# Kernel optimization log

Measured on AMD Instinct MI355X. Metric: run time of the kernel, lower is better.

The kernel has to match this reference:

```python
import jax, jax.numpy as jnp
import numpy as np

PAD, BOS, EOS = 0, 1, 2
VOCAB, EMB, HID, N, T = 32, 32, 512, 4096, 64


def _lstm_step(x, h, c, W_ih, W_hh, b_ih, b_hh):
    # PyTorch nn.LSTM single step; gate order [i|f|g|o]
    g = x @ W_ih.T + h @ W_hh.T + b_ih + b_hh  # [n, 4H]
    i, f, gg, o = jnp.split(g, 4, axis=-1)
    i = jax.nn.sigmoid(i)
    f = jax.nn.sigmoid(f)
    gg = jnp.tanh(gg)
    o = jax.nn.sigmoid(o)
    c = f * c + i * gg
    h = o * jnp.tanh(c)
    return h, c


def setup_inputs() -> dict:
    key = jax.random.key(0)
    ks = jax.random.split(key, 12)
    s = 0.04  # ~1/sqrt(hidden), matches torch LSTM init scale
    emb = jax.random.normal(ks[0], (VOCAB, EMB), jnp.float32) * s
    emb = emb.at[PAD].set(0.0)  # padding_idx row is zero
    inp = {
        "prevs": jnp.full((N, 1), BOS, dtype=jnp.int32),
        "emb": emb,
        "W_ih0": jax.random.normal(ks[1], (4 * HID, EMB), jnp.float32) * s,
        "W_hh0": jax.random.normal(ks[2], (4 * HID, HID), jnp.float32) * s,
        "b_ih0": jax.random.normal(ks[3], (4 * HID,), jnp.float32) * s,
        "b_hh0": jax.random.normal(ks[4], (4 * HID,), jnp.float32) * s,
        "W_ih1": jax.random.normal(ks[5], (4 * HID, HID), jnp.float32) * s,
        "W_hh1": jax.random.normal(ks[6], (4 * HID, HID), jnp.float32) * s,
        "b_ih1": jax.random.normal(ks[7], (4 * HID,), jnp.float32) * s,
        "b_hh1": jax.random.normal(ks[8], (4 * HID,), jnp.float32) * s,
        "W_out": jax.random.normal(ks[9], (VOCAB, HID), jnp.float32) * s,
        "b_out": jax.random.normal(ks[10], (VOCAB,), jnp.float32) * s,
        "max_length": T,
    }
    return inp


def reference(prevs, emb, W_ih0, W_hh0, b_ih0, b_hh0,
              W_ih1, W_hh1, b_ih1, b_hh1, W_out, b_out, max_length):
    # softmax+multinomial sampling, <eos>/<pad> bookkeeping.
    n = prevs.shape[0]
    H = W_hh0.shape[1]
    keys = jax.random.split(jax.random.key(7), max_length)
    tok0 = prevs[:, 0]
    h0 = jnp.zeros((n, H), emb.dtype)
    init = (tok0, h0, h0, h0, h0,
            tok0 == EOS, jnp.zeros((n,), jnp.int32))

    def step(carry, key):
        tok, h0, c0, h1, c1, is_end, lengths = carry
        x = emb[tok]                                   # [n, EMB]
        h0, c0 = _lstm_step(x, h0, c0, W_ih0, W_hh0, b_ih0, b_hh0)
        h1, c1 = _lstm_step(h0, h1, c1, W_ih1, W_hh1, b_ih1, b_hh1)
        logits = h1 @ W_out.T + b_out                  # [n, VOCAB]
        sampled = jax.random.categorical(key, logits)  # == multinomial(softmax)
        cur = jnp.where(is_end, PAD, sampled).astype(tok.dtype)
        lengths = lengths + (~is_end).astype(jnp.int32)
        is_end = is_end | (cur == EOS)
        return (cur, h0, c0, h1, c1, is_end, lengths), cur

    carry, toks = jax.lax.scan(step, init, keys)       # toks: [T, n]
    lengths = carry[-1] + 1                            # +1 for <bos>
    samples = jnp.concatenate([prevs, toks.T], axis=1)  # [n, 1+T]
    return samples, lengths
```

## Files before the change

kernel.cpp:

```cpp
#include <hip/hip_runtime.h>
#include <cstdint>
#include <cmath>

#define RNG_VARIANT 1

#define NROWS 4096
#define HIDN 512
#define G4 2048
#define VOC 32
#define TSTEPS 64
#define PAD_TOK 0
#define BOS_TOK 1
#define EOS_TOK 2

__host__ __device__ inline void tf2x32(unsigned k0, unsigned k1, unsigned x0, unsigned x1,
                                       unsigned& o0, unsigned& o1) {
  unsigned ks0 = k0, ks1 = k1, ks2 = k0 ^ k1 ^ 0x1BD11BDAu;
  unsigned X0 = x0 + ks0, X1 = x1 + ks1;
  const unsigned R[5][4] = {{13,15,26,6},{17,29,16,24},{13,15,26,6},{17,29,16,24},{13,15,26,6}};
  unsigned inj0[5], inj1[5];
  inj0[0] = ks1; inj1[0] = ks2;
  inj0[1] = ks2; inj1[1] = ks0;
  inj0[2] = ks0; inj1[2] = ks1;
  inj0[3] = ks1; inj1[3] = ks2;
  inj0[4] = ks2; inj1[4] = ks0;
#pragma unroll
  for (int i = 0; i < 5; ++i) {
#pragma unroll
    for (int j = 0; j < 4; ++j) {
      X0 += X1;
      unsigned r = R[i][j];
      X1 = (X1 << r) | (X1 >> (32 - r));
      X1 ^= X0;
    }
    X0 += inj0[i];
    X1 += inj1[i] + (unsigned)(i + 1);
  }
  o0 = X0; o1 = X1;
}

#define BM 128
#define BN 128
#define BK 32
#define LDP 132

__global__ __launch_bounds__(256) void lstm_gemm(
    const float* __restrict__ A0, const float* __restrict__ B0,
    const float* __restrict__ A1, const float* __restrict__ B1,
    int nparts, float* __restrict__ C)
{
  __shared__ float As[BK][LDP];
  __shared__ float Bs[BK][LDP];
  const int tid = threadIdx.x;
  const int tx = tid & 15, ty = tid >> 4;
  const int m0 = blockIdx.y * BM, n0 = blockIdx.x * BN;
  const int lrow = tid >> 3;
  const int lcol = (tid & 7) << 2;
  float acc[8][8];
#pragma unroll
  for (int i = 0; i < 8; ++i)
#pragma unroll
    for (int j = 0; j < 8; ++j) acc[i][j] = 0.f;

  for (int part = 0; part < nparts; ++part) {
    const float* __restrict__ A = part ? A1 : A0;
    const float* __restrict__ B = part ? B1 : B0;
    for (int kt = 0; kt < HIDN / BK; ++kt) {
      const int kb = kt * BK;
#pragma unroll
      for (int p = 0; p < 4; ++p) {
        const int r = lrow + 32 * p;
        float4 va = *reinterpret_cast<const float4*>(A + (size_t)(m0 + r) * HIDN + kb + lcol);
        float4 vb = *reinterpret_cast<const float4*>(B + (size_t)(n0 + r) * HIDN + kb + lcol);
        As[lcol + 0][r] = va.x; As[lcol + 1][r] = va.y; As[lcol + 2][r] = va.z; As[lcol + 3][r] = va.w;
        Bs[lcol + 0][r] = vb.x; Bs[lcol + 1][r] = vb.y; Bs[lcol + 2][r] = vb.z; Bs[lcol + 3][r] = vb.w;
      }
      __syncthreads();
#pragma unroll
      for (int k = 0; k < BK; ++k) {
        float a[8], b[8];
        *reinterpret_cast<float4*>(&a[0]) = *reinterpret_cast<const float4*>(&As[k][ty * 8]);
        *reinterpret_cast<float4*>(&a[4]) = *reinterpret_cast<const float4*>(&As[k][ty * 8 + 4]);
        *reinterpret_cast<float4*>(&b[0]) = *reinterpret_cast<const float4*>(&Bs[k][tx * 8]);
        *reinterpret_cast<float4*>(&b[4]) = *reinterpret_cast<const float4*>(&Bs[k][tx * 8 + 4]);
#pragma unroll
        for (int i = 0; i < 8; ++i)
#pragma unroll
          for (int j = 0; j < 8; ++j)
            acc[i][j] = fmaf(a[i], b[j], acc[i][j]);
      }
      __syncthreads();
    }
  }
#pragma unroll
  for (int i = 0; i < 8; ++i) {
    float4 v0 = make_float4(acc[i][0], acc[i][1], acc[i][2], acc[i][3]);
    float4 v1 = make_float4(acc[i][4], acc[i][5], acc[i][6], acc[i][7]);
    float* cp = C + (size_t)(m0 + ty * 8 + i) * G4 + n0 + tx * 8;
    *reinterpret_cast<float4*>(cp) = v0;
    *reinterpret_cast<float4*>(cp + 4) = v1;
  }
}

__global__ void lstm_act(const float* __restrict__ gates,
                         const float* __restrict__ extra,
                         const int* __restrict__ tok,
                         float* __restrict__ h, float* __restrict__ c)
{
  const int n = blockIdx.x;
  const int j = blockIdx.y * 256 + threadIdx.x;
  const float* ex = extra + (tok ? (size_t)tok[n] * G4 : 0);
  const size_t base = (size_t)n * G4;
  float gi = gates[base + j]        + ex[j];
  float gf = gates[base + j + 512]  + ex[j + 512];
  float gg = gates[base + j + 1024] + ex[j + 1024];
  float go = gates[base + j + 1536] + ex[j + 1536];
  float si = 1.f / (1.f + expf(-gi));
  float sf = 1.f / (1.f + expf(-gf));
  float tg = tanhf(gg);
  float so = 1.f / (1.f + expf(-go));
  const size_t hi = (size_t)n * HIDN + j;
  float cn = sf * c[hi] + si * tg;
  c[hi] = cn;
  h[hi] = so * tanhf(cn);
}

__global__ void build_ew0(const float* __restrict__ emb, const float* __restrict__ W_ih0,
                          const float* __restrict__ b_ih0, const float* __restrict__ b_hh0,
                          float* __restrict__ EW0)
{
  int idx = blockIdx.x * 256 + threadIdx.x;
  int vv = idx >> 11, j = idx & 2047;
  float s = b_ih0[j] + b_hh0[j];
#pragma unroll
  for (int e = 0; e < 32; ++e)
    s = fmaf(emb[vv * 32 + e], W_ih0[(size_t)j * 32 + e], s);
  EW0[idx] = s;
}

__global__ void add_bias(const float* __restrict__ a, const float* __restrict__ b,
                         float* __restrict__ o) {
  int j = blockIdx.x * 256 + threadIdx.x;
  if (j < G4) o[j] = a[j] + b[j];
}

__global__ void init_state(const int* __restrict__ prevs, int* __restrict__ tok,
                           int* __restrict__ is_end, int* __restrict__ lengths,
                           int* __restrict__ out)
{
  int n = blockIdx.x * 256 + threadIdx.x;
  if (n < NROWS) {
    int p = prevs[n];
    tok[n] = p;
    is_end[n] = (p == EOS_TOK) ? 1 : 0;
    lengths[n] = 0;
    out[(size_t)n * (TSTEPS + 1)] = p;
  }
}

__global__ __launch_bounds__(64) void sample_step(
    const float* __restrict__ h1, const float* __restrict__ W_out,
    const float* __restrict__ b_out,
    int* __restrict__ tok, int* __restrict__ is_end, int* __restrict__ lengths,
    int* __restrict__ out, unsigned key0, unsigned key1, int t, int last)
{
  __shared__ float hrow[HIDN];
  const int n = blockIdx.x;
  const int lane = threadIdx.x;
  {
    const float4* src = reinterpret_cast<const float4*>(h1 + (size_t)n * HIDN);
    float4* dst = reinterpret_cast<float4*>(hrow);
    dst[lane] = src[lane];
    dst[lane + 64] = src[lane + 64];
  }
  __syncthreads();
  const int v = lane & 31, half = lane >> 5;
  const float* w  = W_out + (size_t)v * HIDN + half * 256;
  const float* hh = hrow + half * 256;
  float dot = 0.f;
#pragma unroll
  for (int k = 0; k < 256; k += 4) {
    float4 wv = *reinterpret_cast<const float4*>(w + k);
    float4 hv = *reinterpret_cast<const float4*>(hh + k);
    dot = fmaf(wv.x, hv.x, dot);
    dot = fmaf(wv.y, hv.y, dot);
    dot = fmaf(wv.z, hv.z, dot);
    dot = fmaf(wv.w, hv.w, dot);
  }
  dot += __shfl_xor(dot, 32);
  const float logit = dot + b_out[v];

  const unsigned iflat = (unsigned)(n * 32 + v);
  unsigned r0, r1, bits;
#if RNG_VARIANT == 1
  tf2x32(key0, key1, 0u, iflat, r0, r1);
  bits = r0 ^ r1;
#elif RNG_VARIANT == 2
  if (iflat < 65536u) { tf2x32(key0, key1, iflat, iflat + 65536u, r0, r1); bits = r0; }
  else                { tf2x32(key0, key1, iflat - 65536u, iflat, r0, r1); bits = r1; }
#else
  tf2x32(key0, key1, 0u, iflat, r0, r1);
  bits = r1;
#endif
  float f = __uint_as_float((bits >> 9) | 0x3f800000u) - 1.0f;
  float u = fmaxf(f, 1.1754943508222875e-38f);
  float t1 = -(float)log((double)u);
  float g  = -(float)log((double)t1);
  float s = g + logit;

  float bs = s; int bi = v;
#pragma unroll
  for (int off = 16; off >= 1; off >>= 1) {
    float os = __shfl_xor(bs, off);
    int   oi = __shfl_xor(bi, off);
    if (os > bs || (os == bs && oi < bi)) { bs = os; bi = oi; }
  }
  if (lane == 0) {
    const int oe  = is_end[n];
    const int cur = oe ? PAD_TOK : bi;
    const int len = lengths[n] + (oe ? 0 : 1);
    lengths[n] = len;
    is_end[n] = (oe || (cur == EOS_TOK)) ? 1 : 0;
    tok[n] = cur;
    out[(size_t)n * (TSTEPS + 1) + t + 1] = cur;
    if (last) out[(size_t)NROWS * (TSTEPS + 1) + n] = len + 1;
  }
}

extern "C" void kernel_launch(void* const* d_in, const int* in_sizes, int n_in,
                              void* d_out, int out_size, void* d_ws, size_t ws_size,
                              hipStream_t stream)
{
  const int*   prevs = (const int*)d_in[0];
  const float* emb   = (const float*)d_in[1];
  const float* W_ih0 = (const float*)d_in[2];
  const float* W_hh0 = (const float*)d_in[3];
  const float* b_ih0 = (const float*)d_in[4];
  const float* b_hh0 = (const float*)d_in[5];
  const float* W_ih1 = (const float*)d_in[6];
  const float* W_hh1 = (const float*)d_in[7];
  const float* b_ih1 = (const float*)d_in[8];
  const float* b_hh1 = (const float*)d_in[9];
  const float* W_out = (const float*)d_in[10];
  const float* b_out = (const float*)d_in[11];

  float* h0    = (float*)d_ws;
  float* c0    = h0 + (size_t)NROWS * HIDN;
  float* h1    = c0 + (size_t)NROWS * HIDN;
  float* c1    = h1 + (size_t)NROWS * HIDN;
  float* gates = c1 + (size_t)NROWS * HIDN;
  float* EW0   = gates + (size_t)NROWS * G4;
  float* bias1 = EW0 + (size_t)VOC * G4;
  int* tok     = (int*)(bias1 + G4);
  int* is_end  = tok + NROWS;
  int* lengths = is_end + NROWS;
  int* outp    = (int*)d_out;

  hipMemsetAsync(h0, 0, (size_t)4 * NROWS * HIDN * sizeof(float), stream);
  init_state<<<NROWS / 256, 256, 0, stream>>>(prevs, tok, is_end, lengths, outp);
  build_ew0<<<VOC * G4 / 256, 256, 0, stream>>>(emb, W_ih0, b_ih0, b_hh0, EW0);
  add_bias<<<G4 / 256, 256, 0, stream>>>(b_ih1, b_hh1, bias1);

  unsigned keys[TSTEPS][2];
#if RNG_VARIANT == 2
  {
    unsigned outv[2 * TSTEPS];
    for (int j = 0; j < TSTEPS; ++j) {
      unsigned o0, o1;
      tf2x32(0u, 7u, (unsigned)j, (unsigned)(j + TSTEPS), o0, o1);
      outv[j] = o0; outv[j + TSTEPS] = o1;
    }
    for (int t = 0; t < TSTEPS; ++t) { keys[t][0] = outv[2 * t]; keys[t][1] = outv[2 * t + 1]; }
  }
#else
  for (int t = 0; t < TSTEPS; ++t) {
    unsigned o0, o1;
    tf2x32(0u, 7u, 0u, (unsigned)t, o0, o1);
    keys[t][0] = o0; keys[t][1] = o1;
  }
#endif

  dim3 ggrid(G4 / BN, NROWS / BM);
  for (int t = 0; t < TSTEPS; ++t) {
    lstm_gemm<<<ggrid, 256, 0, stream>>>(h0, W_hh0, nullptr, nullptr, 1, gates);
    lstm_act<<<dim3(NROWS, 2), 256, 0, stream>>>(gates, EW0, tok, h0, c0);
    lstm_gemm<<<ggrid, 256, 0, stream>>>(h0, W_ih1, h1, W_hh1, 2, gates);
    lstm_act<<<dim3(NROWS, 2), 256, 0, stream>>>(gates, bias1, nullptr, h1, c1);
    sample_step<<<NROWS, 64, 0, stream>>>(h1, W_out, b_out, tok, is_end, lengths, outp,
                                          keys[t][0], keys[t][1], t, t == TSTEPS - 1);
  }
}
```

Baseline: 22.42 ms.

## Fuse LSTM gate GEMM with activation using interleaved gate columns and LDS double-buffering

Replaces the separate gate GEMM and activation kernels with one fused kernel per layer. Each block computes the i/f/g/o columns for 32 hidden units, so the cell update runs in registers and the full gates tensor is never written or read back. The kernel stages A/B tiles directly into LDS with global_load_lds in a double-buffered loop. h buffers are ping-ponged because blocks now read h while other blocks write it, and the bias/embedding tables are stored in interleaved gate order. The cost is 4-byte-granular async loads and a less regular B-row access pattern.

After: 35.47 ms. +58.2%, slower.

```diff
diff --git a/kernel.cpp b/kernel.cpp
--- a/kernel.cpp
+++ b/kernel.cpp
@@ -6,12 +6,18 @@
 
 #define NROWS 4096
 #define HIDN 512
-#define G4 2048
 #define VOC 32
 #define TSTEPS 64
 #define PAD_TOK 0
 #define BOS_TOK 1
 #define EOS_TOK 2
+
+#define BK 32
+#define BM 128
+#define JJT 32
+
+typedef const __attribute__((address_space(1))) unsigned int* gptr_t;
+typedef __attribute__((address_space(3))) unsigned int* lptr_t;
 
 __host__ __device__ inline void tf2x32(unsigned k0, unsigned k1, unsigned x0, unsigned x1,
                                        unsigned& o0, unsigned& o1) {
@@ -39,95 +45,126 @@
   o0 = X0; o1 = X1;
 }
 
-#define BM 128
-#define BN 128
-#define BK 32
-#define LDP 132
-
-__global__ __launch_bounds__(256) void lstm_gemm(
+template<int NPARTS, bool LAYER0>
+__global__ __launch_bounds__(256, 2) void lstm_fused(
     const float* __restrict__ A0, const float* __restrict__ B0,
     const float* __restrict__ A1, const float* __restrict__ B1,
-    int nparts, float* __restrict__ C)
-{
-  __shared__ float As[BK][LDP];
-  __shared__ float Bs[BK][LDP];
+    const float* __restrict__ extra,
+    const int* __restrict__ tokv,
+    float* __restrict__ h, float* __restrict__ c)
+{
+  __shared__ float As[2][BK * BM];
+  __shared__ float Bs[2][BK * BM];
   const int tid = threadIdx.x;
-  const int tx = tid & 15, ty = tid >> 4;
-  const int m0 = blockIdx.y * BM, n0 = blockIdx.x * BN;
-  const int lrow = tid >> 3;
-  const int lcol = (tid & 7) << 2;
+  const int lane = tid & 63;
+  const int w = tid >> 6;
+  const int wr = w >> 1, wc = w & 1;
+  const int ty = lane >> 3, tx = lane & 7;
+  const int m0 = blockIdx.y * BM;
+  const int c0 = blockIdx.x * JJT;
+  const int kA = w * 8;
+
+  const size_t arow0 = (size_t)(m0 + lane) * HIDN;
+  const size_t arow1 = (size_t)(m0 + 64 + lane) * HIDN;
+  const size_t brow0 = (size_t)((lane & 3) * HIDN + c0 + (lane >> 2)) * HIDN;
+  const size_t brow1 = brow0 + (size_t)16 * HIDN;
+
   float acc[8][8];
 #pragma unroll
   for (int i = 0; i < 8; ++i)
 #pragma unroll
     for (int j = 0; j < 8; ++j) acc[i][j] = 0.f;
 
-  for (int part = 0; part < nparts; ++part) {
-    const float* __restrict__ A = part ? A1 : A0;
-    const float* __restrict__ B = part ? B1 : B0;
-    for (int kt = 0; kt < HIDN / BK; ++kt) {
-      const int kb = kt * BK;
-#pragma unroll
-      for (int p = 0; p < 4; ++p) {
-        const int r = lrow + 32 * p;
-        float4 va = *reinterpret_cast<const float4*>(A + (size_t)(m0 + r) * HIDN + kb + lcol);
-        float4 vb = *reinterpret_cast<const float4*>(B + (size_t)(n0 + r) * HIDN + kb + lcol);
-        As[lcol + 0][r] = va.x; As[lcol + 1][r] = va.y; As[lcol + 2][r] = va.z; As[lcol + 3][r] = va.w;
-        Bs[lcol + 0][r] = vb.x; Bs[lcol + 1][r] = vb.y; Bs[lcol + 2][r] = vb.z; Bs[lcol + 3][r] = vb.w;
-      }
-      __syncthreads();
-#pragma unroll
-      for (int k = 0; k < BK; ++k) {
-        float a[8], b[8];
-        *reinterpret_cast<float4*>(&a[0]) = *reinterpret_cast<const float4*>(&As[k][ty * 8]);
-        *reinterpret_cast<float4*>(&a[4]) = *reinterpret_cast<const float4*>(&As[k][ty * 8 + 4]);
-        *reinterpret_cast<float4*>(&b[0]) = *reinterpret_cast<const float4*>(&Bs[k][tx * 8]);
-        *reinterpret_cast<float4*>(&b[4]) = *reinterpret_cast<const float4*>(&Bs[k][tx * 8 + 4]);
-#pragma unroll
-        for (int i = 0; i < 8; ++i)
-#pragma unroll
-          for (int j = 0; j < 8; ++j)
-            acc[i][j] = fmaf(a[i], b[j], acc[i][j]);
-      }
-      __syncthreads();
+  const int NT = NPARTS * (HIDN / BK);
+
+  auto STAGE = [&](int tt, int sel) {
+    const float* A = A0;
+    const float* B = B0;
+    if (NPARTS == 2 && (tt >> 4)) { A = A1; B = B1; }
+    const int kb = (tt & 15) * BK;
+    float* dA = &As[sel][0];
+    float* dB = &Bs[sel][0];
+#pragma unroll
+    for (int i = 0; i < 16; ++i) {
+      const int k = kA + (i >> 1);
+      const float* sA = A + ((i & 1) ? arow1 : arow0) + (size_t)(kb + k);
+      const float* sB = B + ((i & 1) ? brow1 : brow0) + (size_t)(kb + k);
+      __builtin_amdgcn_global_load_lds((gptr_t)sA, (lptr_t)(dA + k * BM + (i & 1) * 64), 4, 0, 0);
+      __builtin_amdgcn_global_load_lds((gptr_t)sB, (lptr_t)(dB + k * BM + (i & 1) * 64), 4, 0, 0);
     }
+  };
+
+  STAGE(0, 0);
+  __syncthreads();
+  int sel = 0;
+  for (int tt = 0; tt < NT; ++tt) {
+    if (tt + 1 < NT) STAGE(tt + 1, sel ^ 1);
+    const float* aP = &As[sel][wr * 64 + ty * 8];
+    const float* bP = &Bs[sel][wc * 64 + tx * 8];
+#pragma unroll
+    for (int k = 0; k < BK; ++k) {
+      float4 a0 = *(const float4*)(aP + k * BM);
+      float4 a1 = *(const float4*)(aP + k * BM + 4);
+      float4 b0 = *(const float4*)(bP + k * BM);
+      float4 b1 = *(const float4*)(bP + k * BM + 4);
+      const float av[8] = {a0.x, a0.y, a0.z, a0.w, a1.x, a1.y, a1.z, a1.w};
+      const float bv[8] = {b0.x, b0.y, b0.z, b0.w, b1.x, b1.y, b1.z, b1.w};
+#pragma unroll
+      for (int i2 = 0; i2 < 8; ++i2)
+#pragma unroll
+        for (int j2 = 0; j2 < 8; ++j2)
+          acc[i2][j2] = fmaf(av[i2], bv[j2], acc[i2][j2]);
+    }
+    __syncthreads();
+    sel ^= 1;
+  }
+
+  const int jjl = wc * 16 + tx * 2;
+  const size_t colb = (size_t)(c0 + jjl);
+  float e[8];
+  if (!LAYER0) {
+    float4 e0 = *(const float4*)(extra + colb * 4);
+    float4 e1 = *(const float4*)(extra + colb * 4 + 4);
+    e[0] = e0.x; e[1] = e0.y; e[2] = e0.z; e[3] = e0.w;
+    e[4] = e1.x; e[5] = e1.y; e[6] = e1.z; e[7] = e1.w;
   }
 #pragma unroll
   for (int i = 0; i < 8; ++i) {
-    float4 v0 = make_float4(acc[i][0], acc[i][1], acc[i][2], acc[i][3]);
-    float4 v1 = make_float4(acc[i][4], acc[i][5], acc[i][6], acc[i][7]);
-    float* cp = C + (size_t)(m0 + ty * 8 + i) * G4 + n0 + tx * 8;
-    *reinterpret_cast<float4*>(cp) = v0;
-    *reinterpret_cast<float4*>(cp + 4) = v1;
-  }
-}
-
-__global__ void lstm_act(const float* __restrict__ gates,
-                         const float* __restrict__ extra,
-                         const int* __restrict__ tok,
-                         float* __restrict__ h, float* __restrict__ c)
-{
-  const int n = blockIdx.x;
-  const int j = blockIdx.y * 256 + threadIdx.x;
-  const float* ex = extra + (tok ? (size_t)tok[n] * G4 : 0);
-  const size_t base = (size_t)n * G4;
-  float gi = gates[base + j]        + ex[j];
-  float gf = gates[base + j + 512]  + ex[j + 512];
-  float gg = gates[base + j + 1024] + ex[j + 1024];
-  float go = gates[base + j + 1536] + ex[j + 1536];
-  float si = 1.f / (1.f + expf(-gi));
-  float sf = 1.f / (1.f + expf(-gf));
-  float tg = tanhf(gg);
-  float so = 1.f / (1.f + expf(-go));
-  const size_t hi = (size_t)n * HIDN + j;
-  float cn = sf * c[hi] + si * tg;
-  c[hi] = cn;
-  h[hi] = so * tanhf(cn);
+    const int n = m0 + wr * 64 + ty * 8 + i;
+    if (LAYER0) {
+      const int tk = tokv[n];
+      const float* ex = extra + (size_t)tk * 2048 + colb * 4;
+      float4 e0 = *(const float4*)(ex);
+      float4 e1 = *(const float4*)(ex + 4);
+      e[0] = e0.x; e[1] = e0.y; e[2] = e0.z; e[3] = e0.w;
+      e[4] = e1.x; e[5] = e1.y; e[6] = e1.z; e[7] = e1.w;
+    }
+    float gi0 = acc[i][0] + e[0], gf0 = acc[i][1] + e[1];
+    float gg0 = acc[i][2] + e[2], go0 = acc[i][3] + e[3];
+    float gi1 = acc[i][4] + e[4], gf1 = acc[i][5] + e[5];
+    float gg1 = acc[i][6] + e[6], go1 = acc[i][7] + e[7];
+    const size_t idx = (size_t)n * HIDN + colb;
+    float2 cold = *(const float2*)(c + idx);
+    float si0 = 1.f / (1.f + expf(-gi0));
+    float sf0 = 1.f / (1.f + expf(-gf0));
+    float tg0 = tanhf(gg0);
+    float so0 = 1.f / (1.f + expf(-go0));
+    float cn0 = sf0 * cold.x + si0 * tg0;
+    float hn0 = so0 * tanhf(cn0);
+    float si1 = 1.f / (1.f + expf(-gi1));
+    float sf1 = 1.f / (1.f + expf(-gf1));
+    float tg1 = tanhf(gg1);
+    float so1 = 1.f / (1.f + expf(-go1));
+    float cn1 = sf1 * cold.y + si1 * tg1;
+    float hn1 = so1 * tanhf(cn1);
+    *(float2*)(c + idx) = make_float2(cn0, cn1);
+    *(float2*)(h + idx) = make_float2(hn0, hn1);
+  }
 }
 
 __global__ void build_ew0(const float* __restrict__ emb, const float* __restrict__ W_ih0,
                           const float* __restrict__ b_ih0, const float* __restrict__ b_hh0,
-                          float* __restrict__ EW0)
+                          float* __restrict__ EW0i)
 {
   int idx = blockIdx.x * 256 + threadIdx.x;
   int vv = idx >> 11, j = idx & 2047;
@@ -135,13 +172,13 @@
 #pragma unroll
   for (int e = 0; e < 32; ++e)
     s = fmaf(emb[vv * 32 + e], W_ih0[(size_t)j * 32 + e], s);
-  EW0[idx] = s;
-}
-
-__global__ void add_bias(const float* __restrict__ a, const float* __restrict__ b,
-                         float* __restrict__ o) {
+  EW0i[(size_t)vv * 2048 + (size_t)(j & 511) * 4 + (j >> 9)] = s;
+}
+
+__global__ void build_bias1i(const float* __restrict__ a, const float* __restrict__ b,
+                             float* __restrict__ o) {
   int j = blockIdx.x * 256 + threadIdx.x;
-  if (j < G4) o[j] = a[j] + b[j];
+  o[(size_t)(j & 511) * 4 + (j >> 9)] = a[j] + b[j];
 }
 
 __global__ void init_state(const int* __restrict__ prevs, int* __restrict__ tok,
@@ -175,12 +212,12 @@
   }
   __syncthreads();
   const int v = lane & 31, half = lane >> 5;
-  const float* w  = W_out + (size_t)v * HIDN + half * 256;
+  const float* wp = W_out + (size_t)v * HIDN + half * 256;
   const float* hh = hrow + half * 256;
   float dot = 0.f;
 #pragma unroll
   for (int k = 0; k < 256; k += 4) {
-    float4 wv = *reinterpret_cast<const float4*>(w + k);
+    float4 wv = *reinterpret_cast<const float4*>(wp + k);
     float4 hv = *reinterpret_cast<const float4*>(hh + k);
     dot = fmaf(wv.x, hv.x, dot);
     dot = fmaf(wv.y, hv.y, dot);
@@ -244,49 +281,43 @@
   const float* W_out = (const float*)d_in[10];
   const float* b_out = (const float*)d_in[11];
 
-  float* h0    = (float*)d_ws;
-  float* c0    = h0 + (size_t)NROWS * HIDN;
-  float* h1    = c0 + (size_t)NROWS * HIDN;
-  float* c1    = h1 + (size_t)NROWS * HIDN;
-  float* gates = c1 + (size_t)NROWS * HIDN;
-  float* EW0   = gates + (size_t)NROWS * G4;
-  float* bias1 = EW0 + (size_t)VOC * G4;
-  int* tok     = (int*)(bias1 + G4);
+  const size_t S = (size_t)NROWS * HIDN;
+  float* h0a   = (float*)d_ws;
+  float* h1a   = h0a + S;
+  float* cl0   = h1a + S;
+  float* cl1   = cl0 + S;
+  float* h0b   = cl1 + S;
+  float* h1b   = h0b + S;
+  float* EW0i  = h1b + S;
+  float* bias1i = EW0i + (size_t)VOC * 2048;
+  int* tok     = (int*)(bias1i + 2048);
   int* is_end  = tok + NROWS;
   int* lengths = is_end + NROWS;
   int* outp    = (int*)d_out;
 
-  hipMemsetAsync(h0, 0, (size_t)4 * NROWS * HIDN * sizeof(float), stream);
+  hipMemsetAsync(h0a, 0, 4 * S * sizeof(float), stream);
   init_state<<<NROWS / 256, 256, 0, stream>>>(prevs, tok, is_end, lengths, outp);
-  build_ew0<<<VOC * G4 / 256, 256, 0, stream>>>(emb, W_ih0, b_ih0, b_hh0, EW0);
-  add_bias<<<G4 / 256, 256, 0, stream>>>(b_ih1, b_hh1, bias1);
+  build_ew0<<<VOC * 2048 / 256, 256, 0, stream>>>(emb, W_ih0, b_ih0, b_hh0, EW0i);
+  build_bias1i<<<2048 / 256, 256, 0, stream>>>(b_ih1, b_hh1, bias1i);
 
   unsigned keys[TSTEPS][2];
-#if RNG_VARIANT == 2
-  {
-    unsigned outv[2 * TSTEPS];
-    for (int j = 0; j < TSTEPS; ++j) {
-      unsigned o0, o1;
-      tf2x32(0u, 7u, (unsigned)j, (unsigned)(j + TSTEPS), o0, o1);
-      outv[j] = o0; outv[j + TSTEPS] = o1;
-    }
-    for (int t = 0; t < TSTEPS; ++t) { keys[t][0] = outv[2 * t]; keys[t][1] = outv[2 * t + 1]; }
-  }
-#else
   for (int t = 0; t < TSTEPS; ++t) {
     unsigned o0, o1;
     tf2x32(0u, 7u, 0u, (unsigned)t, o0, o1);
     keys[t][0] = o0; keys[t][1] = o1;
   }
-#endif
-
-  dim3 ggrid(G4 / BN, NROWS / BM);
+
+  dim3 ggrid(HIDN / JJT, NROWS / BM);
   for (int t = 0; t < TSTEPS; ++t) {
-    lstm_gemm<<<ggrid, 256, 0, stream>>>(h0, W_hh0, nullptr, nullptr, 1, gates);
-    lstm_act<<<dim3(NROWS, 2), 256, 0, stream>>>(gates, EW0, tok, h0, c0);
-    lstm_gemm<<<ggrid, 256, 0, stream>>>(h0, W_ih1, h1, W_hh1, 2, gates);
-    lstm_act<<<dim3(NROWS, 2), 256, 0, stream>>>(gates, bias1, nullptr, h1, c1);
-    sample_step<<<NROWS, 64, 0, stream>>>(h1, W_out, b_out, tok, is_end, lengths, outp,
+    float* h0rd = (t & 1) ? h0b : h0a;
+    float* h0wr = (t & 1) ? h0a : h0b;
+    float* h1rd = (t & 1) ? h1b : h1a;
+    float* h1wr = (t & 1) ? h1a : h1b;
+    lstm_fused<1, true><<<ggrid, 256, 0, stream>>>(
+        h0rd, W_hh0, nullptr, nullptr, EW0i, tok, h0wr, cl0);
+    lstm_fused<2, false><<<ggrid, 256, 0, stream>>>(
+        h0wr, W_ih1, h1rd, W_hh1, bias1i, nullptr, h1wr, cl1);
+    sample_step<<<NROWS, 64, 0, stream>>>(h1wr, W_out, b_out, tok, is_end, lengths, outp,
                                           keys[t][0], keys[t][1], t, t == TSTEPS - 1);
   }
 }
```
